# Performance work log

Hardware: AMD Instinct MI355X
Metric: run time of the kernel (lower is better)

The kernel has to match this reference:

```python
import jax, jax.numpy as jnp
import numpy as np

H = 12        # num_attention_heads
D = 768       # hidden_size
DH = D // H   # attention_size per head (64)
B, S = 1, 4096


def setup_inputs() -> dict:
    key = jax.random.key(0)
    ks = jax.random.split(key, 10)
    scale = 0.02
    x = jax.random.normal(ks[0], (B, S, D), dtype=jnp.float32)
    # per-head QKV weights stacked: [H, D, DH]
    wq = jax.random.normal(ks[1], (H, D, DH), dtype=jnp.float32) * scale
    wk = jax.random.normal(ks[2], (H, D, DH), dtype=jnp.float32) * scale
    wv = jax.random.normal(ks[3], (H, D, DH), dtype=jnp.float32) * scale
    bq = jax.random.normal(ks[4], (H, DH), dtype=jnp.float32) * scale
    bk = jax.random.normal(ks[5], (H, DH), dtype=jnp.float32) * scale
    bv = jax.random.normal(ks[6], (H, DH), dtype=jnp.float32) * scale
    wo = jax.random.normal(ks[7], (D, D), dtype=jnp.float32) * scale
    bo = jax.random.normal(ks[8], (D,), dtype=jnp.float32) * scale
    return {"x": x, "wq": wq, "bq": bq, "wk": wk, "bk": bk,
            "wv": wv, "bv": bv, "wo": wo, "bo": bo}


def reference(x, wq, bq, wk, bk, wv, bv, wo, bo):
    # per-head linear projections: [B,S,D] x [H,D,DH] -> [B,H,S,DH]
    q = jnp.einsum('bsd,hde->bhse', x, wq) + bq[None, :, None, :]
    k = jnp.einsum('bsd,hde->bhse', x, wk) + bk[None, :, None, :]
    v = jnp.einsum('bsd,hde->bhse', x, wv) + bv[None, :, None, :]
    # scaled dot-product attention, full NxN probs as in original
    scores = jnp.einsum('bhse,bhte->bhst', q, k) / jnp.sqrt(jnp.float32(DH))
    probs = jax.nn.softmax(scores, axis=-1)          # [B,H,S,S]
    ctx = jnp.einsum('bhst,bhte->bhse', probs, v)    # [B,H,S,DH]
    # concat heads along feature dim (head order = original ModuleList order)
    ctx = jnp.transpose(ctx, (0, 2, 1, 3)).reshape(B, S, H * DH)
    out = ctx @ wo + bo                               # output projection
    return out
```

## Files before the change

kernel.cpp:

```cpp
#include <hip/hip_runtime.h>


using frag8 = __attribute__((ext_vector_type(8))) short;
using facc4 = __attribute__((ext_vector_type(4))) float;
using uint4v = __attribute__((ext_vector_type(4))) unsigned int;

#define LOG2E 1.4426950408889634f
#define THR_LOG2 11.5415603f
#define SWZ16(r, b) ((b) ^ (((r) & 7) << 4))

#if defined(__has_builtin)
#  if __has_builtin(__builtin_amdgcn_exp2f)
#    define EXP2(x) __builtin_amdgcn_exp2f(x)
#  else
#    define EXP2(x) exp2f(x)
#  endif
#else
#  define EXP2(x) exp2f(x)
#endif

__device__ __forceinline__ unsigned short f2bf(float f) {
  unsigned int u = __builtin_bit_cast(unsigned int, f);
  u = (u + 0x7FFFu + ((u >> 16) & 1u)) >> 16;
  return (unsigned short)u;
}
__device__ __forceinline__ float bf2f(unsigned short s) {
  unsigned int u = ((unsigned int)s) << 16;
  return __builtin_bit_cast(float, u);
}
__device__ __forceinline__ unsigned cvt_pk_bf16(float lo, float hi) {
  unsigned r;
  asm("v_cvt_pk_bf16_f32 %0, %1, %2" : "=v"(r) : "v"(lo), "v"(hi));
  return r;
}

__device__ __forceinline__ facc4 mfma_bf16(frag8 a, frag8 b, facc4 c) {
  return __builtin_amdgcn_mfma_f32_16x16x32_bf16(a, b, c, 0, 0, 0);
}

__device__ __forceinline__ void gld_lds16(const void* g, void* l) {
  auto gp = (const __attribute__((address_space(1))) unsigned int*)g;
  auto lp = (__attribute__((address_space(3))) unsigned int*)l;
  __builtin_amdgcn_global_load_lds(gp, lp, 16, 0, 0);
}

__global__ __launch_bounds__(256) void k_cvt_x(const float* __restrict__ in,
                                               unsigned short* __restrict__ out) {
  int i = (blockIdx.x * 256 + threadIdx.x) * 8;
  float4 a = *(const float4*)(in + i);
  float4 b = *(const float4*)(in + i + 4);
  frag8 r;
  r[0] = (short)f2bf(a.x); r[1] = (short)f2bf(a.y);
  r[2] = (short)f2bf(a.z); r[3] = (short)f2bf(a.w);
  r[4] = (short)f2bf(b.x); r[5] = (short)f2bf(b.y);
  r[6] = (short)f2bf(b.z); r[7] = (short)f2bf(b.w);
  *(frag8*)(out + i) = r;
}

__global__ __launch_bounds__(256) void k_prep_w(
    const float* __restrict__ wq, const float* __restrict__ wk,
    const float* __restrict__ wv, const float* __restrict__ wo,
    unsigned short* __restrict__ wqT, unsigned short* __restrict__ wkT,
    unsigned short* __restrict__ wvT, unsigned short* __restrict__ woT) {
  __shared__ unsigned short tile[64][65];
  const int bx = blockIdx.x;
  const float* src; unsigned short* dst;
  int ld_src, ld_dst, r0, c0;
  if (bx < 432) {
    int p = bx / 144, rem = bx % 144;
    int h = rem / 12, dt = rem % 12;
    src = (p == 0 ? wq : (p == 1 ? wk : wv)) + (size_t)h * 768 * 64;
    dst = (p == 0 ? wqT : (p == 1 ? wkT : wvT)) + (size_t)h * 64 * 768;
    ld_src = 64; ld_dst = 768; r0 = dt * 64; c0 = 0;
  } else {
    int t = bx - 432;
    src = wo; dst = woT;
    ld_src = 768; ld_dst = 768;
    r0 = (t / 12) * 64; c0 = (t % 12) * 64;
  }
  const int tid = threadIdx.x;
  const int lr = tid >> 2, lc0 = (tid & 3) * 16;
#pragma unroll
  for (int i = 0; i < 16; ++i)
    tile[lr][lc0 + i] = f2bf(src[(size_t)(r0 + lr) * ld_src + c0 + lc0 + i]);
  __syncthreads();
  const int oc = tid >> 2;
#pragma unroll
  for (int i = 0; i < 16; ++i)
    dst[(size_t)(c0 + oc) * ld_dst + r0 + lc0 + i] = tile[lc0 + i][oc];
}

__global__ __launch_bounds__(256) void k_qkv(
    const unsigned short* __restrict__ xb, const unsigned short* __restrict__ wT,
    const float* __restrict__ bq, const float* __restrict__ bk,
    const float* __restrict__ bv,
    unsigned short* __restrict__ qo, unsigned short* __restrict__ ko,
    unsigned short* __restrict__ vTo) {
  __shared__ __align__(16) unsigned short As[128 * 72];
  __shared__ __align__(16) unsigned short Bs[64 * 72];
  const int sb = blockIdx.x, ph = blockIdx.y;
  const int p = ph / 12, h = ph % 12;
  const int s0 = sb * 128;
  const int tid = threadIdx.x;
  const int w = tid >> 6, l = tid & 63;
  const int lg = l >> 4, li = l & 15;
  const int wm = w >> 1, wn = w & 1;
  const unsigned short* wTb = wT + (size_t)ph * 64 * 768;

  facc4 acc[4][2];
#pragma unroll
  for (int i = 0; i < 4; ++i)
#pragma unroll
    for (int j = 0; j < 2; ++j) acc[i][j] = (facc4){0.f, 0.f, 0.f, 0.f};

  const int rA = tid >> 3;
  const int c8 = (tid & 7) * 8;

  for (int k0 = 0; k0 < 768; k0 += 64) {
    frag8 av[4], bw[2];
#pragma unroll
    for (int i = 0; i < 4; ++i)
      av[i] = *(const frag8*)(xb + (size_t)(s0 + i * 32 + rA) * 768 + k0 + c8);
#pragma unroll
    for (int i = 0; i < 2; ++i)
      bw[i] = *(const frag8*)(wTb + (size_t)(i * 32 + rA) * 768 + k0 + c8);
#pragma unroll
    for (int i = 0; i < 4; ++i)
      *(frag8*)(&As[(i * 32 + rA) * 72 + c8]) = av[i];
#pragma unroll
    for (int i = 0; i < 2; ++i)
      *(frag8*)(&Bs[(i * 32 + rA) * 72 + c8]) = bw[i];
    __syncthreads();
#pragma unroll
    for (int kk = 0; kk < 2; ++kk) {
      const int ce = kk * 32 + lg * 8;
      frag8 a[4], b[2];
#pragma unroll
      for (int mf = 0; mf < 4; ++mf)
        a[mf] = *(const frag8*)(&As[(wm * 64 + mf * 16 + li) * 72 + ce]);
#pragma unroll
      for (int nf = 0; nf < 2; ++nf)
        b[nf] = *(const frag8*)(&Bs[(wn * 32 + nf * 16 + li) * 72 + ce]);
#pragma unroll
      for (int mf = 0; mf < 4; ++mf)
#pragma unroll
        for (int nf = 0; nf < 2; ++nf)
          acc[mf][nf] = mfma_bf16(a[mf], b[nf], acc[mf][nf]);
    }
    __syncthreads();
  }

  const float* bias = (p == 0 ? bq : (p == 1 ? bk : bv)) + h * 64;
  const float scale = (p == 0) ? 0.125f * LOG2E : 1.0f;
  float bvv[2];
#pragma unroll
  for (int nf = 0; nf < 2; ++nf) bvv[nf] = bias[wn * 32 + nf * 16 + li];
#pragma unroll
  for (int mf = 0; mf < 4; ++mf)
#pragma unroll
    for (int nf = 0; nf < 2; ++nf) {
      int e = wn * 32 + nf * 16 + li;
#pragma unroll
      for (int j = 0; j < 4; ++j) {
        int s = s0 + wm * 64 + mf * 16 + lg * 4 + j;
        unsigned short bf = f2bf((acc[mf][nf][j] + bvv[nf]) * scale);
        if (p == 0)      qo[((size_t)h * 4096 + s) * 64 + e] = bf;
        else if (p == 1) ko[((size_t)h * 4096 + s) * 64 + e] = bf;
        else             vTo[((size_t)h * 64 + e) * 4096 + s] = bf;
      }
    }
}

__global__ __launch_bounds__(512) void k_attn(
    const unsigned short* __restrict__ q, const unsigned short* __restrict__ k,
    const unsigned short* __restrict__ vT,
    unsigned short* __restrict__ oP, float* __restrict__ mlP) {
  __shared__ __align__(16) char Kb[2][8192];
  __shared__ __align__(16) char Vb[2][8192];
  const int bid = blockIdx.x;
  const int part = blockIdx.y;
  const int h = bid >> 5, qb = bid & 31;
  const int s0 = qb * 128;
  const int tid = threadIdx.x;
  const int w = tid >> 6, l = tid & 63;
  const int lg = l >> 4, li = l & 15;
  const unsigned short* Kh = k + (size_t)h * 4096 * 64;
  const unsigned short* Vh = vT + (size_t)h * 64 * 4096;

  const int rS = tid >> 3;
  const int bS = (tid & 7) * 16;
  const int sbS = SWZ16(rS, bS);

  const unsigned short* qrow = q + ((size_t)h * 4096 + s0 + w * 16 + li) * 64;
  frag8 qf0 = *(const frag8*)(qrow + lg * 8);
  frag8 qf1 = *(const frag8*)(qrow + 32 + lg * 8);

  const int a_ = li >> 2, b_ = li & 3;
  const int r_base = 8 * a_ + b_;
  const int par4 = (a_ & 1) * 4;

  float m = -1e30f, lsum = 0.f;
  facc4 acc[4];
#pragma unroll
  for (int nf = 0; nf < 4; ++nf) acc[nf] = (facc4){0.f, 0.f, 0.f, 0.f};

  const int kb0 = part * 2048;

  gld_lds16((const char*)(Kh + (size_t)(kb0 + rS) * 64) + sbS, Kb[0] + w * 1024);
  gld_lds16((const char*)(Vh + (size_t)rS * 4096 + kb0) + sbS, Vb[0] + w * 1024);
  __syncthreads();

  int cur = 0;
  for (int kt = 0; kt < 32; ++kt) {
    if (kt < 31) {
      const int kbn = kb0 + (kt + 1) * 64;
      gld_lds16((const char*)(Kh + (size_t)(kbn + rS) * 64) + sbS,
                Kb[cur ^ 1] + w * 1024);
      gld_lds16((const char*)(Vh + (size_t)rS * 4096 + kbn) + sbS,
                Vb[cur ^ 1] + w * 1024);
    }
    const char* Kc = Kb[cur];
    const char* Vc = Vb[cur];

    facc4 sf[4];
#pragma unroll
    for (int cn = 0; cn < 4; ++cn) {
      int r = r_base + (((cn & 1) == 0) ? par4 : (4 - par4 > 0 ? 4 - 4 * (a_ & 1) : 0));
      r = r_base + 4 * ((cn & 1) ^ (a_ & 1)) + 32 * (cn >> 1);
      frag8 a0 = *(const frag8*)(Kc + r * 128 + SWZ16(r, lg * 16));
      frag8 a1 = *(const frag8*)(Kc + r * 128 + SWZ16(r, 64 + lg * 16));
      facc4 s = (facc4){0.f, 0.f, 0.f, 0.f};
      s = mfma_bf16(a0, qf0, s);
      s = mfma_bf16(a1, qf1, s);
      sf[cn] = s;
    }
    if (lg & 1) {
      facc4 t = sf[0]; sf[0] = sf[1]; sf[1] = t;
      t = sf[2]; sf[2] = sf[3]; sf[3] = t;
    }
    float t0 = fmaxf(fmaxf(fmaxf(sf[0][0], sf[0][1]), fmaxf(sf[0][2], sf[0][3])),
                     fmaxf(fmaxf(sf[1][0], sf[1][1]), fmaxf(sf[1][2], sf[1][3])));
    float t1 = fmaxf(fmaxf(fmaxf(sf[2][0], sf[2][1]), fmaxf(sf[2][2], sf[2][3])),
                     fmaxf(fmaxf(sf[3][0], sf[3][1]), fmaxf(sf[3][2], sf[3][3])));
    float tmax = fmaxf(t0, t1);
    tmax = fmaxf(tmax, __shfl_xor(tmax, 16));
    tmax = fmaxf(tmax, __shfl_xor(tmax, 32));
    if (__any(tmax > m + THR_LOG2)) {
      float mn = fmaxf(m, tmax);
      float corr = EXP2(m - mn);
      m = mn;
      lsum *= corr;
#pragma unroll
      for (int j = 0; j < 4; ++j) {
        float cj = __shfl(corr, (l & 48) | (4 * lg + j));
#pragma unroll
        for (int nf = 0; nf < 4; ++nf) acc[nf][j] *= cj;
      }
    }
    float pv[4][4];
#pragma unroll
    for (int cn = 0; cn < 4; ++cn)
#pragma unroll
      for (int j = 0; j < 4; ++j) {
        pv[cn][j] = EXP2(sf[cn][j] - m);
        lsum += pv[cn][j];
      }
    uint4v u0, u1;
    u0[0] = cvt_pk_bf16(pv[0][0], pv[0][1]);
    u0[1] = cvt_pk_bf16(pv[0][2], pv[0][3]);
    u0[2] = cvt_pk_bf16(pv[1][0], pv[1][1]);
    u0[3] = cvt_pk_bf16(pv[1][2], pv[1][3]);
    u1[0] = cvt_pk_bf16(pv[2][0], pv[2][1]);
    u1[1] = cvt_pk_bf16(pv[2][2], pv[2][3]);
    u1[2] = cvt_pk_bf16(pv[3][0], pv[3][1]);
    u1[3] = cvt_pk_bf16(pv[3][2], pv[3][3]);
    frag8 pa0 = __builtin_bit_cast(frag8, u0);
    frag8 pa1 = __builtin_bit_cast(frag8, u1);
#pragma unroll
    for (int nf = 0; nf < 4; ++nf) {
      int rv = nf * 16 + li;
      frag8 vb0 = *(const frag8*)(Vc + rv * 128 + SWZ16(rv, lg * 16));
      frag8 vb1 = *(const frag8*)(Vc + rv * 128 + SWZ16(rv, 64 + lg * 16));
      acc[nf] = mfma_bf16(pa0, vb0, acc[nf]);
      acc[nf] = mfma_bf16(pa1, vb1, acc[nf]);
    }
    __syncthreads();
    cur ^= 1;
  }
  lsum += __shfl_xor(lsum, 16);
  lsum += __shfl_xor(lsum, 32);
  const size_t base = ((size_t)(part * 12 + h) * 4096 + s0 + w * 16);
  float Lj[4];
#pragma unroll
  for (int j = 0; j < 4; ++j)
    Lj[j] = __shfl(lsum, (l & 48) | (4 * lg + j));
#pragma unroll
  for (int nf = 0; nf < 4; ++nf)
#pragma unroll
    for (int j = 0; j < 4; ++j)
      oP[(base + lg * 4 + j) * 64 + nf * 16 + li] = f2bf(acc[nf][j] / Lj[j]);
  if (lg == 0) {
    mlP[(base + li) * 2 + 0] = m;
    mlP[(base + li) * 2 + 1] = lsum;
  }
}

__global__ __launch_bounds__(256) void k_combine(
    const unsigned short* __restrict__ oP, const float* __restrict__ mlP,
    unsigned short* __restrict__ ctx) {
  const int tid = threadIdx.x;
  const int rg = blockIdx.x * 4 + (tid >> 6);
  const int e = tid & 63;
  const int h = rg >> 12, s = rg & 4095;
  const size_t r0 = (size_t)h * 4096 + s;
  const size_t r1 = (size_t)(12 + h) * 4096 + s;
  float m0 = mlP[r0 * 2], l0 = mlP[r0 * 2 + 1];
  float m1 = mlP[r1 * 2], l1 = mlP[r1 * 2 + 1];
  float M = fmaxf(m0, m1);
  float w0 = l0 * EXP2(m0 - M);
  float w1 = l1 * EXP2(m1 - M);
  float inv = 1.f / (w0 + w1);
  float o = (w0 * bf2f(oP[r0 * 64 + e]) + w1 * bf2f(oP[r1 * 64 + e])) * inv;
  ctx[(size_t)s * 768 + h * 64 + e] = f2bf(o);
}

__global__ __launch_bounds__(256) void k_proj(
    const unsigned short* __restrict__ ctx, const unsigned short* __restrict__ woT,
    const float* __restrict__ bo, float* __restrict__ out) {
  __shared__ __align__(16) unsigned short As[64 * 72];
  __shared__ __align__(16) unsigned short Bs[64 * 72];
  const int s0 = blockIdx.x * 64, j0 = blockIdx.y * 64;
  const int tid = threadIdx.x;
  const int w = tid >> 6, l = tid & 63;
  const int lg = l >> 4, li = l & 15;
  const int wm = w >> 1, wn = w & 1;
  facc4 acc[2][2];
#pragma unroll
  for (int i = 0; i < 2; ++i)
#pragma unroll
    for (int j = 0; j < 2; ++j) acc[i][j] = (facc4){0.f, 0.f, 0.f, 0.f};

  const int rA = tid >> 3;
  const int c8 = (tid & 7) * 8;

  for (int k0 = 0; k0 < 768; k0 += 64) {
    frag8 av[2], bw[2];
#pragma unroll
    for (int i = 0; i < 2; ++i) {
      av[i] = *(const frag8*)(ctx + (size_t)(s0 + i * 32 + rA) * 768 + k0 + c8);
      bw[i] = *(const frag8*)(woT + (size_t)(j0 + i * 32 + rA) * 768 + k0 + c8);
    }
#pragma unroll
    for (int i = 0; i < 2; ++i) {
      *(frag8*)(&As[(i * 32 + rA) * 72 + c8]) = av[i];
      *(frag8*)(&Bs[(i * 32 + rA) * 72 + c8]) = bw[i];
    }
    __syncthreads();
#pragma unroll
    for (int kk = 0; kk < 2; ++kk) {
      const int ce = kk * 32 + lg * 8;
      frag8 a[2], b[2];
#pragma unroll
      for (int mf = 0; mf < 2; ++mf)
        a[mf] = *(const frag8*)(&As[(wm * 32 + mf * 16 + li) * 72 + ce]);
#pragma unroll
      for (int nf = 0; nf < 2; ++nf)
        b[nf] = *(const frag8*)(&Bs[(wn * 32 + nf * 16 + li) * 72 + ce]);
#pragma unroll
      for (int mf = 0; mf < 2; ++mf)
#pragma unroll
        for (int nf = 0; nf < 2; ++nf)
          acc[mf][nf] = mfma_bf16(a[mf], b[nf], acc[mf][nf]);
    }
    __syncthreads();
  }
#pragma unroll
  for (int nf = 0; nf < 2; ++nf) {
    int jc = j0 + wn * 32 + nf * 16 + li;
    float bb = bo[jc];
#pragma unroll
    for (int mf = 0; mf < 2; ++mf)
#pragma unroll
      for (int j = 0; j < 4; ++j) {
        int s = s0 + wm * 32 + mf * 16 + lg * 4 + j;
        out[(size_t)s * 768 + jc] = acc[mf][nf][j] + bb;
      }
  }
}

extern "C" void kernel_launch(void* const* d_in, const int* in_sizes, int n_in,
                              void* d_out, int out_size, void* d_ws, size_t ws_size,
                              hipStream_t stream) {
  const float* x  = (const float*)d_in[0];
  const float* wq = (const float*)d_in[1];
  const float* bq = (const float*)d_in[2];
  const float* wk = (const float*)d_in[3];
  const float* bk = (const float*)d_in[4];
  const float* wv = (const float*)d_in[5];
  const float* bv = (const float*)d_in[6];
  const float* wo = (const float*)d_in[7];
  const float* bo = (const float*)d_in[8];
  float* out = (float*)d_out;

  char* ws = (char*)d_ws;
  unsigned short* xb  = (unsigned short*)(ws);
  unsigned short* wT  = (unsigned short*)(ws + 6291456);
  unsigned short* woT = (unsigned short*)(ws + 9830400);
  unsigned short* qd  = (unsigned short*)(ws + 11010048);
  unsigned short* kd  = (unsigned short*)(ws + 17301504);
  unsigned short* vTd = (unsigned short*)(ws + 23592960);
  unsigned short* ctx = (unsigned short*)(ws + 29884416);
  unsigned short* oP  = (unsigned short*)(ws + 36175872);
  float*          mlP = (float*)(ws + 48758784);

  k_cvt_x<<<1536, 256, 0, stream>>>(x, xb);
  k_prep_w<<<576, 256, 0, stream>>>(wq, wk, wv, wo,
                                    wT, wT + 589824, wT + 1179648, woT);
  k_qkv<<<dim3(32, 36), 256, 0, stream>>>(xb, wT, bq, bk, bv, qd, kd, vTd);
  k_attn<<<dim3(384, 2), 512, 0, stream>>>(qd, kd, vTd, oP, mlP);
  k_combine<<<12288, 256, 0, stream>>>(oP, mlP, ctx);
  k_proj<<<dim3(64, 12), 256, 0, stream>>>(ctx, woT, bo, out);
}
```

Measured before the change: 141.8 us.

## Use direct global-to-LDS swizzled loads in GEMMs and MFMA row-sum in attention

The QKV and output-projection GEMMs now copy their tiles straight from global memory into LDS with the gld_lds16 path and an XOR swizzle, replacing the register-staged copy into padded rows. This removes the VGPR round-trip and shrinks LDS use. In the attention kernel, the softmax denominator is now accumulated by an MFMA against a ones vector instead of scalar adds plus shuffles, and the max reduction is rewritten as a chain of fmaxf calls. The extra MFMA work per tile trades matrix-core time for fewer VALU operations and shuffles. The swizzle layout must match the gld_lds16 lane mapping for results to stay correct.

```diff
diff --git a/kernel.cpp b/kernel.cpp
--- a/kernel.cpp
+++ b/kernel.cpp
@@ -96,8 +96,8 @@
     const float* __restrict__ bv,
     unsigned short* __restrict__ qo, unsigned short* __restrict__ ko,
     unsigned short* __restrict__ vTo) {
-  __shared__ __align__(16) unsigned short As[128 * 72];
-  __shared__ __align__(16) unsigned short Bs[64 * 72];
+  __shared__ __align__(16) unsigned short As[128 * 64];
+  __shared__ __align__(16) unsigned short Bs[64 * 64];
   const int sb = blockIdx.x, ph = blockIdx.y;
   const int p = ph / 12, h = ph % 12;
   const int s0 = sb * 128;
@@ -114,33 +114,36 @@
     for (int j = 0; j < 2; ++j) acc[i][j] = (facc4){0.f, 0.f, 0.f, 0.f};
 
   const int rA = tid >> 3;
-  const int c8 = (tid & 7) * 8;
+  const int cbp = (tid & 7) * 16;
 
   for (int k0 = 0; k0 < 768; k0 += 64) {
-    frag8 av[4], bw[2];
-#pragma unroll
-    for (int i = 0; i < 4; ++i)
-      av[i] = *(const frag8*)(xb + (size_t)(s0 + i * 32 + rA) * 768 + k0 + c8);
-#pragma unroll
-    for (int i = 0; i < 2; ++i)
-      bw[i] = *(const frag8*)(wTb + (size_t)(i * 32 + rA) * 768 + k0 + c8);
-#pragma unroll
-    for (int i = 0; i < 4; ++i)
-      *(frag8*)(&As[(i * 32 + rA) * 72 + c8]) = av[i];
-#pragma unroll
-    for (int i = 0; i < 2; ++i)
-      *(frag8*)(&Bs[(i * 32 + rA) * 72 + c8]) = bw[i];
+#pragma unroll
+    for (int i = 0; i < 4; ++i) {
+      int r = i * 32 + rA;
+      gld_lds16((const char*)(xb + (size_t)(s0 + r) * 768 + k0) + SWZ16(r, cbp),
+                (char*)As + i * 4096 + w * 1024);
+    }
+#pragma unroll
+    for (int i = 0; i < 2; ++i) {
+      int r = i * 32 + rA;
+      gld_lds16((const char*)(wTb + (size_t)r * 768 + k0) + SWZ16(r, cbp),
+                (char*)Bs + i * 4096 + w * 1024);
+    }
     __syncthreads();
 #pragma unroll
     for (int kk = 0; kk < 2; ++kk) {
-      const int ce = kk * 32 + lg * 8;
+      const int cbl = kk * 64 + lg * 16;
       frag8 a[4], b[2];
 #pragma unroll
-      for (int mf = 0; mf < 4; ++mf)
-        a[mf] = *(const frag8*)(&As[(wm * 64 + mf * 16 + li) * 72 + ce]);
-#pragma unroll
-      for (int nf = 0; nf < 2; ++nf)
-        b[nf] = *(const frag8*)(&Bs[(wn * 32 + nf * 16 + li) * 72 + ce]);
+      for (int mf = 0; mf < 4; ++mf) {
+        int r = wm * 64 + mf * 16 + li;
+        a[mf] = *(const frag8*)((const char*)As + r * 128 + SWZ16(r, cbl));
+      }
+#pragma unroll
+      for (int nf = 0; nf < 2; ++nf) {
+        int r = wn * 32 + nf * 16 + li;
+        b[nf] = *(const frag8*)((const char*)Bs + r * 128 + SWZ16(r, cbl));
+      }
 #pragma unroll
       for (int mf = 0; mf < 4; ++mf)
 #pragma unroll
@@ -195,12 +198,16 @@
   frag8 qf0 = *(const frag8*)(qrow + lg * 8);
   frag8 qf1 = *(const frag8*)(qrow + 32 + lg * 8);
 
+  frag8 onesf;
+#pragma unroll
+  for (int i = 0; i < 8; ++i) onesf[i] = (short)0x3F80;
+
   const int a_ = li >> 2, b_ = li & 3;
   const int r_base = 8 * a_ + b_;
-  const int par4 = (a_ & 1) * 4;
-
-  float m = -1e30f, lsum = 0.f;
+
+  float m = -1e30f;
   facc4 acc[4];
+  facc4 accl = (facc4){0.f, 0.f, 0.f, 0.f};
 #pragma unroll
   for (int nf = 0; nf < 4; ++nf) acc[nf] = (facc4){0.f, 0.f, 0.f, 0.f};
 
@@ -225,8 +232,7 @@
     facc4 sf[4];
 #pragma unroll
     for (int cn = 0; cn < 4; ++cn) {
-      int r = r_base + (((cn & 1) == 0) ? par4 : (4 - par4 > 0 ? 4 - 4 * (a_ & 1) : 0));
-      r = r_base + 4 * ((cn & 1) ^ (a_ & 1)) + 32 * (cn >> 1);
+      int r = r_base + 4 * ((cn & 1) ^ (a_ & 1)) + 32 * (cn >> 1);
       frag8 a0 = *(const frag8*)(Kc + r * 128 + SWZ16(r, lg * 16));
       frag8 a1 = *(const frag8*)(Kc + r * 128 + SWZ16(r, 64 + lg * 16));
       facc4 s = (facc4){0.f, 0.f, 0.f, 0.f};
@@ -238,21 +244,24 @@
       facc4 t = sf[0]; sf[0] = sf[1]; sf[1] = t;
       t = sf[2]; sf[2] = sf[3]; sf[3] = t;
     }
-    float t0 = fmaxf(fmaxf(fmaxf(sf[0][0], sf[0][1]), fmaxf(sf[0][2], sf[0][3])),
-                     fmaxf(fmaxf(sf[1][0], sf[1][1]), fmaxf(sf[1][2], sf[1][3])));
-    float t1 = fmaxf(fmaxf(fmaxf(sf[2][0], sf[2][1]), fmaxf(sf[2][2], sf[2][3])),
-                     fmaxf(fmaxf(sf[3][0], sf[3][1]), fmaxf(sf[3][2], sf[3][3])));
-    float tmax = fmaxf(t0, t1);
+    float t = fmaxf(fmaxf(sf[0][0], sf[0][1]), sf[0][2]);
+    t = fmaxf(fmaxf(t, sf[0][3]), sf[1][0]);
+    t = fmaxf(fmaxf(t, sf[1][1]), sf[1][2]);
+    t = fmaxf(fmaxf(t, sf[1][3]), sf[2][0]);
+    t = fmaxf(fmaxf(t, sf[2][1]), sf[2][2]);
+    t = fmaxf(fmaxf(t, sf[2][3]), sf[3][0]);
+    t = fmaxf(fmaxf(t, sf[3][1]), sf[3][2]);
+    float tmax = fmaxf(t, sf[3][3]);
     tmax = fmaxf(tmax, __shfl_xor(tmax, 16));
     tmax = fmaxf(tmax, __shfl_xor(tmax, 32));
     if (__any(tmax > m + THR_LOG2)) {
       float mn = fmaxf(m, tmax);
       float corr = EXP2(m - mn);
       m = mn;
-      lsum *= corr;
 #pragma unroll
       for (int j = 0; j < 4; ++j) {
         float cj = __shfl(corr, (l & 48) | (4 * lg + j));
+        accl[j] *= cj;
 #pragma unroll
         for (int nf = 0; nf < 4; ++nf) acc[nf][j] *= cj;
       }
@@ -261,10 +270,8 @@
 #pragma unroll
     for (int cn = 0; cn < 4; ++cn)
 #pragma unroll
-      for (int j = 0; j < 4; ++j) {
+      for (int j = 0; j < 4; ++j)
         pv[cn][j] = EXP2(sf[cn][j] - m);
-        lsum += pv[cn][j];
-      }
     uint4v u0, u1;
     u0[0] = cvt_pk_bf16(pv[0][0], pv[0][1]);
     u0[1] = cvt_pk_bf16(pv[0][2], pv[0][3]);
@@ -276,6 +283,8 @@
     u1[3] = cvt_pk_bf16(pv[3][2], pv[3][3]);
     frag8 pa0 = __builtin_bit_cast(frag8, u0);
     frag8 pa1 = __builtin_bit_cast(frag8, u1);
+    accl = mfma_bf16(pa0, onesf, accl);
+    accl = mfma_bf16(pa1, onesf, accl);
 #pragma unroll
     for (int nf = 0; nf < 4; ++nf) {
       int rv = nf * 16 + li;
@@ -287,21 +296,18 @@
     __syncthreads();
     cur ^= 1;
   }
-  lsum += __shfl_xor(lsum, 16);
-  lsum += __shfl_xor(lsum, 32);
   const size_t base = ((size_t)(part * 12 + h) * 4096 + s0 + w * 16);
-  float Lj[4];
-#pragma unroll
-  for (int j = 0; j < 4; ++j)
-    Lj[j] = __shfl(lsum, (l & 48) | (4 * lg + j));
 #pragma unroll
   for (int nf = 0; nf < 4; ++nf)
 #pragma unroll
     for (int j = 0; j < 4; ++j)
-      oP[(base + lg * 4 + j) * 64 + nf * 16 + li] = f2bf(acc[nf][j] / Lj[j]);
-  if (lg == 0) {
+      oP[(base + lg * 4 + j) * 64 + nf * 16 + li] = f2bf(acc[nf][j] / accl[j]);
+  if (lg == 0)
     mlP[(base + li) * 2 + 0] = m;
-    mlP[(base + li) * 2 + 1] = lsum;
+  if (li == 0) {
+#pragma unroll
+    for (int j = 0; j < 4; ++j)
+      mlP[(base + lg * 4 + j) * 2 + 1] = accl[j];
   }
 }
 
@@ -327,8 +333,8 @@
 __global__ __launch_bounds__(256) void k_proj(
     const unsigned short* __restrict__ ctx, const unsigned short* __restrict__ woT,
     const float* __restrict__ bo, float* __restrict__ out) {
-  __shared__ __align__(16) unsigned short As[64 * 72];
-  __shared__ __align__(16) unsigned short Bs[64 * 72];
+  __shared__ __align__(16) unsigned short As[64 * 64];
+  __shared__ __align__(16) unsigned short Bs[64 * 64];
   const int s0 = blockIdx.x * 64, j0 = blockIdx.y * 64;
   const int tid = threadIdx.x;
   const int w = tid >> 6, l = tid & 63;
@@ -341,31 +347,32 @@
     for (int j = 0; j < 2; ++j) acc[i][j] = (facc4){0.f, 0.f, 0.f, 0.f};
 
   const int rA = tid >> 3;
-  const int c8 = (tid & 7) * 8;
+  const int cbp = (tid & 7) * 16;
 
   for (int k0 = 0; k0 < 768; k0 += 64) {
-    frag8 av[2], bw[2];
 #pragma unroll
     for (int i = 0; i < 2; ++i) {
-      av[i] = *(const frag8*)(ctx + (size_t)(s0 + i * 32 + rA) * 768 + k0 + c8);
-      bw[i] = *(const frag8*)(woT + (size_t)(j0 + i * 32 + rA) * 768 + k0 + c8);
-    }
-#pragma unroll
-    for (int i = 0; i < 2; ++i) {
-      *(frag8*)(&As[(i * 32 + rA) * 72 + c8]) = av[i];
-      *(frag8*)(&Bs[(i * 32 + rA) * 72 + c8]) = bw[i];
+      int r = i * 32 + rA;
+      gld_lds16((const char*)(ctx + (size_t)(s0 + r) * 768 + k0) + SWZ16(r, cbp),
+                (char*)As + i * 4096 + w * 1024);
+      gld_lds16((const char*)(woT + (size_t)(j0 + r) * 768 + k0) + SWZ16(r, cbp),
+                (char*)Bs + i * 4096 + w * 1024);
     }
     __syncthreads();
 #pragma unroll
     for (int kk = 0; kk < 2; ++kk) {
-      const int ce = kk * 32 + lg * 8;
+      const int cbl = kk * 64 + lg * 16;
       frag8 a[2], b[2];
 #pragma unroll
-      for (int mf = 0; mf < 2; ++mf)
-        a[mf] = *(const frag8*)(&As[(wm * 32 + mf * 16 + li) * 72 + ce]);
-#pragma unroll
-      for (int nf = 0; nf < 2; ++nf)
-        b[nf] = *(const frag8*)(&Bs[(wn * 32 + nf * 16 + li) * 72 + ce]);
+      for (int mf = 0; mf < 2; ++mf) {
+        int r = wm * 32 + mf * 16 + li;
+        a[mf] = *(const frag8*)((const char*)As + r * 128 + SWZ16(r, cbl));
+      }
+#pragma unroll
+      for (int nf = 0; nf < 2; ++nf) {
+        int r = wn * 32 + nf * 16 + li;
+        b[nf] = *(const frag8*)((const char*)Bs + r * 128 + SWZ16(r, cbl));
+      }
 #pragma unroll
       for (int mf = 0; mf < 2; ++mf)
 #pragma unroll
```

After: 140.4 us. About the same (-1.0%).
